# Performance work log

Hardware: AMD Instinct MI355X
Metric: run time of the kernel (lower is better)

## Reference

```python
import jax, jax.numpy as jnp
import numpy as np

T = 4            # number of node types (len(output_sizes))
N = 16384        # nodes per type
D_IN = 512       # input_size
D_H = 1024       # hidden_size
OUT_SIZES = (128, 96, 64, 32)
MAX_OUT = max(OUT_SIZES)


def setup_inputs() -> dict:
    key = jax.random.key(0)
    ks = jax.random.split(key, 16)
    inp = {}
    for t in range(T):
        inp[f"x{t}"] = jax.random.normal(ks[t], (N, D_IN), jnp.float32)
    # nodes are grouped by type (sorted), matching the padded dict layout
    inp["node_type"] = jnp.repeat(jnp.arange(T, dtype=jnp.int64), N)
    # layer1: per-type Linear(input_size, hidden_size) (apply_net)
    inp["W1"] = jax.random.normal(ks[4], (T, D_IN, D_H), jnp.float32) * 0.02
    inp["b1"] = jnp.zeros((T, D_H), jnp.float32)
    # layer2: per-type Linear(hidden_size, out_size_t)
    for t in range(T):
        inp[f"W2_{t}"] = jax.random.normal(ks[5 + t], (D_H, OUT_SIZES[t]), jnp.float32) * 0.02
        inp[f"b2_{t}"] = jnp.zeros((OUT_SIZES[t],), jnp.float32)
    return inp


def reference(x0, x1, x2, x3, node_type, W1, b1,
              W2_0, b2_0, W2_1, b2_1, W2_2, b2_2, W2_3, b2_3):
    # Per-type gather is implicit: x{t} already holds the features of the
    # nodes whose node_type == t (node_type is sorted/blocked).
    xs = jnp.stack([x0, x1, x2, x3])                       # [T, N, D_IN]
    # apply_net: layer1 per type + activation (batched grouped-GEMM)
    h = jax.nn.relu(jnp.einsum('tni,tih->tnh', xs, W1) + b1[:, None, :])  # [T, N, D_H]
    W2s = (W2_0, W2_1, W2_2, W2_3)
    b2s = (b2_0, b2_1, b2_2, b2_3)
    outs = []
    for t in range(T):  # fixed small set of structurally distinct heads
        o = h[t] @ W2s[t] + b2s[t]                         # [N, out_t]
        outs.append(jnp.pad(o, ((0, 0), (0, MAX_OUT - o.shape[1]))))  # _pad to MAX_OUT
    return jnp.stack(outs)                                 # [T, N, MAX_OUT]
```

## Files before the change

### kernel.cpp

```cpp
#include <hip/hip_runtime.h>
#include <hip/hip_bf16.h>


typedef __attribute__((ext_vector_type(8))) short short8;
typedef __attribute__((ext_vector_type(4))) float f32x4;

#define NT 4
#define NNODE 16384
#define DIN 512
#define DH 1024
#define MAXO 128

static __device__ __forceinline__ ushort f2bf(float f) {
    __hip_bfloat16 h = __float2bfloat16(f);
    return *reinterpret_cast<ushort*>(&h);
}

static __device__ __forceinline__ short8 pack8(const float4 a, const float4 b) {
    union { short8 v; ushort u[8]; } r;
    r.u[0] = f2bf(a.x); r.u[1] = f2bf(a.y); r.u[2] = f2bf(a.z); r.u[3] = f2bf(a.w);
    r.u[4] = f2bf(b.x); r.u[5] = f2bf(b.y); r.u[6] = f2bf(b.z); r.u[7] = f2bf(b.w);
    return r.v;
}

#define GLD(gsrc, ldst)                                                        \
    __builtin_amdgcn_global_load_lds(                                          \
        (const __attribute__((address_space(1))) void*)(gsrc),                 \
        (__attribute__((address_space(3))) void*)(ldst), 16, 0, 0)

__global__ __launch_bounds__(256) void cvt_w_t_kernel(
    const float* __restrict__ in, ushort* __restrict__ out,
    int R, int Cin, size_t in_tstride, size_t out_tstride) {
    __shared__ float tile[32][33];
    const int t = blockIdx.z;
    in += (size_t)t * in_tstride;
    out += (size_t)t * out_tstride;
    const int c0 = blockIdx.x * 32, r0 = blockIdx.y * 32;
    const int cx = threadIdx.x & 31;
    const int ry = threadIdx.x >> 5;
#pragma unroll
    for (int j = 0; j < 4; ++j) {
        int rr = ry + j * 8;
        int c = c0 + cx;
        tile[rr][cx] = (c < Cin) ? in[(size_t)(r0 + rr) * Cin + c] : 0.0f;
    }
    __syncthreads();
#pragma unroll
    for (int j = 0; j < 4; ++j) {
        int cc = ry + j * 8;
        out[(size_t)(c0 + cc) * R + r0 + cx] = f2bf(tile[cx][cc]);
    }
}

__global__ __launch_bounds__(256) void cvt_w2_kernel(
    const float* __restrict__ w0, const float* __restrict__ w1,
    const float* __restrict__ w2, const float* __restrict__ w3,
    const float* __restrict__ c0_, const float* __restrict__ c1_,
    const float* __restrict__ c2_, const float* __restrict__ c3_,
    ushort* __restrict__ out, float* __restrict__ b2p) {
    __shared__ float tile[32][33];
    const int t = blockIdx.z;
    const int Cin = (t == 0) ? 128 : (t == 1) ? 96 : (t == 2) ? 64 : 32;
    const float* in = (t == 0) ? w0 : (t == 1) ? w1 : (t == 2) ? w2 : w3;
    ushort* o = out + (size_t)t * MAXO * DH;
    const int c0 = blockIdx.x * 32, r0 = blockIdx.y * 32;
    const int cx = threadIdx.x & 31;
    const int ry = threadIdx.x >> 5;
#pragma unroll
    for (int j = 0; j < 4; ++j) {
        int rr = ry + j * 8;
        int c = c0 + cx;
        tile[rr][cx] = (c < Cin) ? in[(size_t)(r0 + rr) * Cin + c] : 0.0f;
    }
    __syncthreads();
#pragma unroll
    for (int j = 0; j < 4; ++j) {
        int cc = ry + j * 8;
        o[(size_t)(c0 + cc) * DH + r0 + cx] = f2bf(tile[cx][cc]);
    }
    if (blockIdx.x == 0 && blockIdx.y == 0 && threadIdx.x < 128) {
        const float* b = (t == 0) ? c0_ : (t == 1) ? c1_ : (t == 2) ? c2_ : c3_;
        const int n = threadIdx.x;
        b2p[t * 128 + n] = (n < Cin) ? b[n] : 0.0f;
    }
}

template <int BN, bool AFP32, bool RELU, bool OUTBF16>
__global__ __launch_bounds__(512, 1) void gemmf(
    const void* __restrict__ A0, const void* __restrict__ A1,
    const void* __restrict__ A2, const void* __restrict__ A3,
    const ushort* __restrict__ Bbase, const float* __restrict__ biasbase,
    void* __restrict__ Cbase, int N, int K, int MT,
    size_t strideA, size_t strideB, size_t strideBias, size_t strideC) {
    constexpr int NF = BN / 64;
    constexpr int NBC = BN * 8 / 512;
    constexpr int ABYTES = 256 * 64 * 2;
    constexpr int BBYTES = BN * 64 * 2;
    constexpr int BUF = ABYTES + BBYTES;
    __shared__ char lds[2 * BUF];
    static_assert(!AFP32 || NBC == 4, "AFP32 path assumes BN=256");

    const int cpx = gridDim.x >> 3;
    const int g = blockIdx.x;
    const int wg = (g & 7) * cpx + (g >> 3);
    const int NTL = N / BN;
    const int t = wg / (MT * NTL);
    const int rmn = wg % (MT * NTL);
    const int m0 = (rmn / NTL) * 256;
    const int n0 = (rmn % NTL) * BN;

    const float* Af = (const float*)((t == 0) ? A0 : (t == 1) ? A1
                                   : (t == 2) ? A2 : A3);
    const ushort* Ab = (const ushort*)A0 + (size_t)t * strideA;
    const ushort* Bp = Bbase + (size_t)t * strideB;
    const float* bias = biasbase + (size_t)t * strideBias;

    const int tid = threadIdx.x;
    const int lane = tid & 63;
    const int w = tid >> 6;
    const int wm = w >> 2, wn = w & 3;
    const int lrow = lane & 15, lgrp = lane >> 4;

    const float* af32src[4];
    const ushort* abfsrc[4];
    int adst[4];
#pragma unroll
    for (int j = 0; j < 4; ++j) {
        const int c = j * 512 + tid;
        const int r = c >> 3;
        const int c8 = c & 7;
        const int cb = (c8 * 16) ^ ((r & 7) << 4);
        if (AFP32) {
            af32src[j] = Af + (size_t)(m0 + r) * K + c8 * 8;
            adst[j] = r * 128 + cb;
        } else {
            abfsrc[j] = Ab + (size_t)(m0 + r) * K + (cb >> 1);
            adst[j] = c * 16;
        }
    }
    const ushort* bsrc[NBC];
    int bdst[NBC];
#pragma unroll
    for (int j = 0; j < NBC; ++j) {
        const int c = j * 512 + tid;
        const int r = c >> 3;
        const int cb = ((c & 7) * 16) ^ ((r & 7) << 4);
        bsrc[j] = Bp + (size_t)(n0 + r) * K + (cb >> 1);
        bdst[j] = ABYTES + c * 16;
    }

    f32x4 acc[8][NF] = {};
    const int NK = K / 64;
    float4 fa[4][2];

    if (AFP32) {
#pragma unroll
        for (int j = 0; j < 4; ++j) {
            fa[j][0] = *reinterpret_cast<const float4*>(af32src[j]);
            fa[j][1] = *reinterpret_cast<const float4*>(af32src[j] + 4);
        }
#pragma unroll
        for (int j = 0; j < NBC; ++j) GLD(bsrc[j], lds + bdst[j]);
        asm volatile("s_waitcnt vmcnt(4)" ::: "memory");
#pragma unroll
        for (int j = 0; j < 4; ++j)
            *reinterpret_cast<short8*>(lds + adst[j]) = pack8(fa[j][0], fa[j][1]);
        asm volatile("" ::: "memory");
        if (NK > 1) {
#pragma unroll
            for (int j = 0; j < 4; ++j) {
                fa[j][0] = *reinterpret_cast<const float4*>(af32src[j] + 64);
                fa[j][1] = *reinterpret_cast<const float4*>(af32src[j] + 68);
            }
        }
        asm volatile("s_waitcnt vmcnt(8) lgkmcnt(0)" ::: "memory");
    } else {
#pragma unroll
        for (int j = 0; j < 4; ++j) GLD(abfsrc[j], lds + adst[j]);
#pragma unroll
        for (int j = 0; j < NBC; ++j) GLD(bsrc[j], lds + bdst[j]);
        asm volatile("s_waitcnt vmcnt(0) lgkmcnt(0)" ::: "memory");
    }
    __builtin_amdgcn_s_barrier();
    asm volatile("" ::: "memory");

    for (int i = 0; i < NK; ++i) {
        const char* cu_ = lds + (i & 1) * BUF;
        char* nx_ = lds + ((i + 1) & 1) * BUF;
        const int ktn = (i + 1) * 64;
        const bool st = (i + 1 < NK);
        const bool st2 = (i + 2 < NK);

        if (st) {
#pragma unroll
            for (int j = 0; j < NBC; ++j) GLD(bsrc[j] + ktn, nx_ + bdst[j]);
            if (AFP32) {
#pragma unroll
                for (int j = 0; j < 4; ++j)
                    *reinterpret_cast<short8*>(nx_ + adst[j]) =
                        pack8(fa[j][0], fa[j][1]);
                asm volatile("" ::: "memory");
                if (st2) {
#pragma unroll
                    for (int j = 0; j < 4; ++j) {
                        fa[j][0] = *reinterpret_cast<const float4*>(
                            af32src[j] + ktn + 64);
                        fa[j][1] = *reinterpret_cast<const float4*>(
                            af32src[j] + ktn + 68);
                    }
                }
            } else {
#pragma unroll
                for (int j = 0; j < 4; ++j) GLD(abfsrc[j] + ktn, nx_ + adst[j]);
            }
        }

#pragma unroll
        for (int kkk = 0; kkk < 2; ++kkk) {
            short8 bfr[NF], af[8];
#pragma unroll
            for (int ni = 0; ni < NF; ++ni) {
                const int br = wn * (NF * 16) + ni * 16 + lrow;
                const int kb = (kkk * 64 + lgrp * 16) ^ ((br & 7) << 4);
                bfr[ni] = *(const short8*)(cu_ + ABYTES + br * 128 + kb);
            }
#pragma unroll
            for (int ml = 0; ml < 8; ++ml) {
                const int ar = wm * 128 + ml * 16 + lrow;
                const int kb = (kkk * 64 + lgrp * 16) ^ ((ar & 7) << 4);
                af[ml] = *(const short8*)(cu_ + ar * 128 + kb);
            }
#pragma unroll
            for (int ml = 0; ml < 8; ++ml)
#pragma unroll
                for (int ni = 0; ni < NF; ++ni)
                    acc[ml][ni] = __builtin_amdgcn_mfma_f32_16x16x32_bf16(
                        bfr[ni], af[ml], acc[ml][ni], 0, 0, 0);
        }

        if (st) {
            if (AFP32 && st2)
                asm volatile("s_waitcnt vmcnt(8) lgkmcnt(0)" ::: "memory");
            else
                asm volatile("s_waitcnt vmcnt(0) lgkmcnt(0)" ::: "memory");
            __builtin_amdgcn_s_barrier();
            asm volatile("" ::: "memory");
        }
    }

    const int wnoff = n0 + wn * (NF * 16);
    const int wmoff = m0 + wm * 128;
#pragma unroll
    for (int ni = 0; ni < NF; ++ni) {
        const int ncol = wnoff + ni * 16 + lgrp * 4;
        const float4 bv = *reinterpret_cast<const float4*>(&bias[ncol]);
#pragma unroll
        for (int mi = 0; mi < 8; ++mi) {
            const int row = wmoff + mi * 16 + lrow;
            float v0 = acc[mi][ni][0] + bv.x;
            float v1 = acc[mi][ni][1] + bv.y;
            float v2 = acc[mi][ni][2] + bv.z;
            float v3 = acc[mi][ni][3] + bv.w;
            if (RELU) {
                v0 = fmaxf(v0, 0.0f); v1 = fmaxf(v1, 0.0f);
                v2 = fmaxf(v2, 0.0f); v3 = fmaxf(v3, 0.0f);
            }
            const size_t base = (size_t)t * strideC + (size_t)row * N + ncol;
            if (OUTBF16) {
                uint2 p;
                p.x = (uint)f2bf(v0) | ((uint)f2bf(v1) << 16);
                p.y = (uint)f2bf(v2) | ((uint)f2bf(v3) << 16);
                *reinterpret_cast<uint2*>(&((ushort*)Cbase)[base]) = p;
            } else {
                float4 p = {v0, v1, v2, v3};
                *reinterpret_cast<float4*>(&((float*)Cbase)[base]) = p;
            }
        }
    }
}

extern "C" void kernel_launch(void* const* d_in, const int* in_sizes, int n_in,
                              void* d_out, int out_size, void* d_ws, size_t ws_size,
                              hipStream_t stream) {
    const float* x0 = (const float*)d_in[0];
    const float* x1 = (const float*)d_in[1];
    const float* x2 = (const float*)d_in[2];
    const float* x3 = (const float*)d_in[3];
    const float* W1 = (const float*)d_in[5];
    const float* b1 = (const float*)d_in[6];
    const float* W2[4] = {(const float*)d_in[7], (const float*)d_in[9],
                          (const float*)d_in[11], (const float*)d_in[13]};
    const float* b2[4] = {(const float*)d_in[8], (const float*)d_in[10],
                          (const float*)d_in[12], (const float*)d_in[14]};

    char* ws = (char*)d_ws;
    ushort* H   = (ushort*)ws;
    ushort* W1T = (ushort*)(ws + 134217728ull);
    ushort* W2T = (ushort*)(ws + 134217728ull + 4194304ull);
    float*  b2p = (float*)(ws + 134217728ull + 4194304ull + 1048576ull);

    cvt_w_t_kernel<<<dim3(32, 16, 4), 256, 0, stream>>>(
        W1, W1T, DIN, DH, (size_t)DIN * DH, (size_t)DH * DIN);
    cvt_w2_kernel<<<dim3(4, 32, 4), 256, 0, stream>>>(
        W2[0], W2[1], W2[2], W2[3], b2[0], b2[1], b2[2], b2[3], W2T, b2p);

    gemmf<256, true, true, true><<<1024, 512, 0, stream>>>(
        x0, x1, x2, x3, W1T, b1, H,
        DH, DIN, NNODE / 256,
        0, (size_t)DH * DIN, (size_t)DH, (size_t)NNODE * DH);

    gemmf<128, false, false, false><<<256, 512, 0, stream>>>(
        H, H, H, H, W2T, b2p, d_out,
        MAXO, DH, NNODE / 256,
        (size_t)NNODE * DH, (size_t)MAXO * DH, (size_t)MAXO,
        (size_t)NNODE * MAXO);
}
```

Before: 153.7 us.

## Restructure layer-1 GEMM into full-width 64-row tiles converting fp32 A once

Replaces the generic templated GEMM with a specialized layer-1 kernel in which each workgroup owns 64 rows by all 1024 hidden columns. Each fp32 input row is read and converted to bf16 only once instead of once per 256-column tile, and the W1 slices are streamed through a large LDS double buffer. The layer-2 GEMM is specialized separately. This trades redundant fp32 A reads and conversions for much more B (weight) traffic per block and a 144KB LDS footprint.

```diff
diff --git a/kernel.cpp b/kernel.cpp
--- a/kernel.cpp
+++ b/kernel.cpp
@@ -85,35 +85,148 @@
     }
 }
 
-template <int BN, bool AFP32, bool RELU, bool OUTBF16>
-__global__ __launch_bounds__(512, 1) void gemmf(
-    const void* __restrict__ A0, const void* __restrict__ A1,
-    const void* __restrict__ A2, const void* __restrict__ A3,
-    const ushort* __restrict__ Bbase, const float* __restrict__ biasbase,
-    void* __restrict__ Cbase, int N, int K, int MT,
-    size_t strideA, size_t strideB, size_t strideBias, size_t strideC) {
-    constexpr int NF = BN / 64;
-    constexpr int NBC = BN * 8 / 512;
-    constexpr int ABYTES = 256 * 64 * 2;
-    constexpr int BBYTES = BN * 64 * 2;
-    constexpr int BUF = ABYTES + BBYTES;
-    __shared__ char lds[2 * BUF];
-    static_assert(!AFP32 || NBC == 4, "AFP32 path assumes BN=256");
+__global__ __launch_bounds__(512, 1) void gemm1p(
+    const float* __restrict__ x0, const float* __restrict__ x1,
+    const float* __restrict__ x2, const float* __restrict__ x3,
+    const ushort* __restrict__ W1T, const float* __restrict__ b1,
+    ushort* __restrict__ H) {
+    constexpr int K = DIN;
+    __shared__ char lds[147456];
 
     const int cpx = gridDim.x >> 3;
     const int g = blockIdx.x;
     const int wg = (g & 7) * cpx + (g >> 3);
-    const int NTL = N / BN;
-    const int t = wg / (MT * NTL);
-    const int rmn = wg % (MT * NTL);
-    const int m0 = (rmn / NTL) * 256;
-    const int n0 = (rmn % NTL) * BN;
-
-    const float* Af = (const float*)((t == 0) ? A0 : (t == 1) ? A1
-                                   : (t == 2) ? A2 : A3);
-    const ushort* Ab = (const ushort*)A0 + (size_t)t * strideA;
-    const ushort* Bp = Bbase + (size_t)t * strideB;
-    const float* bias = biasbase + (size_t)t * strideBias;
+    const int t = wg >> 8;
+    const int m0 = (wg & 255) * 64;
+
+    const float* Af = (t == 0) ? x0 : (t == 1) ? x1 : (t == 2) ? x2 : x3;
+    const ushort* Bt = W1T + (size_t)t * DH * K;
+    const float* bias = b1 + (size_t)t * DH;
+    ushort* Ht = H + (size_t)t * NNODE * DH;
+
+    const int tid = threadIdx.x;
+    const int lane = tid & 63;
+    const int w = tid >> 6;
+    const int lrow = lane & 15, lgrp = lane >> 4;
+
+    const int ar_ = tid >> 3, ac8 = tid & 7;
+    const float* asrc = Af + (size_t)(m0 + ar_) * K + ac8 * 8;
+    const int adst = ar_ * 128 + ((ac8 * 16) ^ ((ar_ & 7) << 4));
+
+    const ushort* bsrc[8];
+    int bdst[8];
+#pragma unroll
+    for (int j = 0; j < 8; ++j) {
+        const int c = j * 512 + tid;
+        const int r = c >> 3;
+        const int cb = ((c & 7) * 16) ^ ((r & 7) << 4);
+        bsrc[j] = Bt + (size_t)r * K + (cb >> 1);
+        bdst[j] = c * 16;
+    }
+
+    f32x4 acc[4][8] = {};
+    float4 fa0, fa1;
+
+    fa0 = *reinterpret_cast<const float4*>(asrc);
+    fa1 = *reinterpret_cast<const float4*>(asrc + 4);
+#pragma unroll
+    for (int j = 0; j < 8; ++j) GLD(bsrc[j], lds + bdst[j]);
+    asm volatile("s_waitcnt vmcnt(8)" ::: "memory");
+    *reinterpret_cast<short8*>(lds + 131072 + adst) = pack8(fa0, fa1);
+    asm volatile("s_waitcnt vmcnt(0) lgkmcnt(0)" ::: "memory");
+    __builtin_amdgcn_s_barrier();
+    asm volatile("" ::: "memory");
+
+#pragma unroll
+    for (int j = 0; j < 16; ++j) {
+        const int k = j >> 1, h = j & 1;
+
+        if (h == 0 && k + 1 < 8) {
+            fa0 = *reinterpret_cast<const float4*>(asrc + (k + 1) * 64);
+            fa1 = *reinterpret_cast<const float4*>(asrc + (k + 1) * 64 + 4);
+        }
+        if (j + 1 < 16) {
+            const int k2 = (j + 1) >> 1, h2 = (j + 1) & 1;
+            const size_t off = (size_t)(h2 * 512) * K + k2 * 64;
+            char* nb = lds + ((j + 1) & 1) * 65536;
+#pragma unroll
+            for (int jj = 0; jj < 8; ++jj) GLD(bsrc[jj] + off, nb + bdst[jj]);
+        }
+        if (h == 1 && k + 1 < 8)
+            *reinterpret_cast<short8*>(
+                lds + 131072 + ((k + 1) & 1) * 8192 + adst) = pack8(fa0, fa1);
+
+        const char* Bl = lds + (j & 1) * 65536;
+        const char* Al = lds + 131072 + (k & 1) * 8192;
+#pragma unroll
+        for (int kkk = 0; kkk < 2; ++kkk) {
+            short8 bfr[4], af[4];
+#pragma unroll
+            for (int ni = 0; ni < 4; ++ni) {
+                const int br = ni * 128 + w * 16 + lrow;
+                const int kb = (kkk * 64 + lgrp * 16) ^ ((br & 7) << 4);
+                bfr[ni] = *(const short8*)(Bl + br * 128 + kb);
+            }
+#pragma unroll
+            for (int ml = 0; ml < 4; ++ml) {
+                const int ar = ml * 16 + lrow;
+                const int kb = (kkk * 64 + lgrp * 16) ^ ((ar & 7) << 4);
+                af[ml] = *(const short8*)(Al + ar * 128 + kb);
+            }
+#pragma unroll
+            for (int ml = 0; ml < 4; ++ml)
+#pragma unroll
+                for (int ni = 0; ni < 4; ++ni)
+                    acc[ml][h * 4 + ni] = __builtin_amdgcn_mfma_f32_16x16x32_bf16(
+                        bfr[ni], af[ml], acc[ml][h * 4 + ni], 0, 0, 0);
+        }
+
+        if (j + 1 < 16) {
+            asm volatile("s_waitcnt vmcnt(0) lgkmcnt(0)" ::: "memory");
+            __builtin_amdgcn_s_barrier();
+            asm volatile("" ::: "memory");
+        }
+    }
+
+#pragma unroll
+    for (int niG = 0; niG < 8; ++niG) {
+        const int ncol = niG * 128 + w * 16 + lgrp * 4;
+        const float4 bv = *reinterpret_cast<const float4*>(&bias[ncol]);
+#pragma unroll
+        for (int ml = 0; ml < 4; ++ml) {
+            const int row = m0 + ml * 16 + lrow;
+            float v0 = fmaxf(acc[ml][niG][0] + bv.x, 0.0f);
+            float v1 = fmaxf(acc[ml][niG][1] + bv.y, 0.0f);
+            float v2 = fmaxf(acc[ml][niG][2] + bv.z, 0.0f);
+            float v3 = fmaxf(acc[ml][niG][3] + bv.w, 0.0f);
+            uint2 p;
+            p.x = (uint)f2bf(v0) | ((uint)f2bf(v1) << 16);
+            p.y = (uint)f2bf(v2) | ((uint)f2bf(v3) << 16);
+            *reinterpret_cast<uint2*>(&Ht[(size_t)row * DH + ncol]) = p;
+        }
+    }
+}
+
+__global__ __launch_bounds__(512, 1) void gemm2k(
+    const ushort* __restrict__ Hbase, const ushort* __restrict__ Bbase,
+    const float* __restrict__ biasbase, float* __restrict__ Cbase,
+    int N, int K, int MT) {
+    constexpr int NF = 2;
+    constexpr int NBC = 2;
+    constexpr int ABYTES = 256 * 64 * 2;
+    constexpr int BBYTES = 128 * 64 * 2;
+    constexpr int BUF = ABYTES + BBYTES;
+    __shared__ char lds[2 * BUF];
+
+    const int cpx = gridDim.x >> 3;
+    const int g = blockIdx.x;
+    const int wg = (g & 7) * cpx + (g >> 3);
+    const int t = wg / MT;
+    const int m0 = (wg % MT) * 256;
+
+    const ushort* A = Hbase + (size_t)t * NNODE * DH;
+    const ushort* Bp = Bbase + (size_t)t * MAXO * DH;
+    const float* bias = biasbase + (size_t)t * MAXO;
 
     const int tid = threadIdx.x;
     const int lane = tid & 63;
@@ -121,22 +234,15 @@
     const int wm = w >> 2, wn = w & 3;
     const int lrow = lane & 15, lgrp = lane >> 4;
 
-    const float* af32src[4];
     const ushort* abfsrc[4];
     int adst[4];
 #pragma unroll
     for (int j = 0; j < 4; ++j) {
         const int c = j * 512 + tid;
         const int r = c >> 3;
-        const int c8 = c & 7;
-        const int cb = (c8 * 16) ^ ((r & 7) << 4);
-        if (AFP32) {
-            af32src[j] = Af + (size_t)(m0 + r) * K + c8 * 8;
-            adst[j] = r * 128 + cb;
-        } else {
-            abfsrc[j] = Ab + (size_t)(m0 + r) * K + (cb >> 1);
-            adst[j] = c * 16;
-        }
+        const int cb = ((c & 7) * 16) ^ ((r & 7) << 4);
+        abfsrc[j] = A + (size_t)(m0 + r) * K + (cb >> 1);
+        adst[j] = c * 16;
     }
     const ushort* bsrc[NBC];
     int bdst[NBC];
@@ -145,42 +251,18 @@
         const int c = j * 512 + tid;
         const int r = c >> 3;
         const int cb = ((c & 7) * 16) ^ ((r & 7) << 4);
-        bsrc[j] = Bp + (size_t)(n0 + r) * K + (cb >> 1);
+        bsrc[j] = Bp + (size_t)r * K + (cb >> 1);
         bdst[j] = ABYTES + c * 16;
     }
 
     f32x4 acc[8][NF] = {};
     const int NK = K / 64;
-    float4 fa[4][2];
-
-    if (AFP32) {
-#pragma unroll
-        for (int j = 0; j < 4; ++j) {
-            fa[j][0] = *reinterpret_cast<const float4*>(af32src[j]);
-            fa[j][1] = *reinterpret_cast<const float4*>(af32src[j] + 4);
-        }
-#pragma unroll
-        for (int j = 0; j < NBC; ++j) GLD(bsrc[j], lds + bdst[j]);
-        asm volatile("s_waitcnt vmcnt(4)" ::: "memory");
-#pragma unroll
-        for (int j = 0; j < 4; ++j)
-            *reinterpret_cast<short8*>(lds + adst[j]) = pack8(fa[j][0], fa[j][1]);
-        asm volatile("" ::: "memory");
-        if (NK > 1) {
-#pragma unroll
-            for (int j = 0; j < 4; ++j) {
-                fa[j][0] = *reinterpret_cast<const float4*>(af32src[j] + 64);
-                fa[j][1] = *reinterpret_cast<const float4*>(af32src[j] + 68);
-            }
-        }
-        asm volatile("s_waitcnt vmcnt(8) lgkmcnt(0)" ::: "memory");
-    } else {
-#pragma unroll
-        for (int j = 0; j < 4; ++j) GLD(abfsrc[j], lds + adst[j]);
-#pragma unroll
-        for (int j = 0; j < NBC; ++j) GLD(bsrc[j], lds + bdst[j]);
-        asm volatile("s_waitcnt vmcnt(0) lgkmcnt(0)" ::: "memory");
-    }
+
+#pragma unroll
+    for (int j = 0; j < 4; ++j) GLD(abfsrc[j], lds + adst[j]);
+#pragma unroll
+    for (int j = 0; j < NBC; ++j) GLD(bsrc[j], lds + bdst[j]);
+    asm volatile("s_waitcnt vmcnt(0)" ::: "memory");
     __builtin_amdgcn_s_barrier();
     asm volatile("" ::: "memory");
 
@@ -189,30 +271,12 @@
         char* nx_ = lds + ((i + 1) & 1) * BUF;
         const int ktn = (i + 1) * 64;
         const bool st = (i + 1 < NK);
-        const bool st2 = (i + 2 < NK);
 
         if (st) {
 #pragma unroll
+            for (int j = 0; j < 4; ++j) GLD(abfsrc[j] + ktn, nx_ + adst[j]);
+#pragma unroll
             for (int j = 0; j < NBC; ++j) GLD(bsrc[j] + ktn, nx_ + bdst[j]);
-            if (AFP32) {
-#pragma unroll
-                for (int j = 0; j < 4; ++j)
-                    *reinterpret_cast<short8*>(nx_ + adst[j]) =
-                        pack8(fa[j][0], fa[j][1]);
-                asm volatile("" ::: "memory");
-                if (st2) {
-#pragma unroll
-                    for (int j = 0; j < 4; ++j) {
-                        fa[j][0] = *reinterpret_cast<const float4*>(
-                            af32src[j] + ktn + 64);
-                        fa[j][1] = *reinterpret_cast<const float4*>(
-                            af32src[j] + ktn + 68);
-                    }
-                }
-            } else {
-#pragma unroll
-                for (int j = 0; j < 4; ++j) GLD(abfsrc[j] + ktn, nx_ + adst[j]);
-            }
         }
 
 #pragma unroll
@@ -239,16 +303,13 @@
         }
 
         if (st) {
-            if (AFP32 && st2)
-                asm volatile("s_waitcnt vmcnt(8) lgkmcnt(0)" ::: "memory");
-            else
-                asm volatile("s_waitcnt vmcnt(0) lgkmcnt(0)" ::: "memory");
+            asm volatile("s_waitcnt vmcnt(0)" ::: "memory");
             __builtin_amdgcn_s_barrier();
             asm volatile("" ::: "memory");
         }
     }
 
-    const int wnoff = n0 + wn * (NF * 16);
+    const int wnoff = wn * (NF * 16);
     const int wmoff = m0 + wm * 128;
 #pragma unroll
     for (int ni = 0; ni < NF; ++ni) {
@@ -257,24 +318,13 @@
 #pragma unroll
         for (int mi = 0; mi < 8; ++mi) {
             const int row = wmoff + mi * 16 + lrow;
-            float v0 = acc[mi][ni][0] + bv.x;
-            float v1 = acc[mi][ni][1] + bv.y;
-            float v2 = acc[mi][ni][2] + bv.z;
-            float v3 = acc[mi][ni][3] + bv.w;
-            if (RELU) {
-                v0 = fmaxf(v0, 0.0f); v1 = fmaxf(v1, 0.0f);
-                v2 = fmaxf(v2, 0.0f); v3 = fmaxf(v3, 0.0f);
-            }
-            const size_t base = (size_t)t * strideC + (size_t)row * N + ncol;
-            if (OUTBF16) {
-                uint2 p;
-                p.x = (uint)f2bf(v0) | ((uint)f2bf(v1) << 16);
-                p.y = (uint)f2bf(v2) | ((uint)f2bf(v3) << 16);
-                *reinterpret_cast<uint2*>(&((ushort*)Cbase)[base]) = p;
-            } else {
-                float4 p = {v0, v1, v2, v3};
-                *reinterpret_cast<float4*>(&((float*)Cbase)[base]) = p;
-            }
+            float4 p;
+            p.x = acc[mi][ni][0] + bv.x;
+            p.y = acc[mi][ni][1] + bv.y;
+            p.z = acc[mi][ni][2] + bv.z;
+            p.w = acc[mi][ni][3] + bv.w;
+            *reinterpret_cast<float4*>(
+                &Cbase[(size_t)t * NNODE * MAXO + (size_t)row * N + ncol]) = p;
         }
     }
 }
@@ -304,14 +354,8 @@
     cvt_w2_kernel<<<dim3(4, 32, 4), 256, 0, stream>>>(
         W2[0], W2[1], W2[2], W2[3], b2[0], b2[1], b2[2], b2[3], W2T, b2p);
 
-    gemmf<256, true, true, true><<<1024, 512, 0, stream>>>(
-        x0, x1, x2, x3, W1T, b1, H,
-        DH, DIN, NNODE / 256,
-        0, (size_t)DH * DIN, (size_t)DH, (size_t)NNODE * DH);
-
-    gemmf<128, false, false, false><<<256, 512, 0, stream>>>(
-        H, H, H, H, W2T, b2p, d_out,
-        MAXO, DH, NNODE / 256,
-        (size_t)NNODE * DH, (size_t)MAXO * DH, (size_t)MAXO,
-        (size_t)NNODE * MAXO);
-}
+    gemm1p<<<1024, 512, 0, stream>>>(x0, x1, x2, x3, W1T, b1, H);
+
+    gemm2k<<<256, 512, 0, stream>>>(H, W2T, b2p, (float*)d_out,
+                                    MAXO, DH, NNODE / 256);
+}
```

Measured after the change: 163.6 us. 1.06x slower.
